# Performance work log

Measured on AMD Instinct MI355X. Metric: run time of the kernel, lower is better.

The kernel has to match this reference:

```python
import jax, jax.numpy as jnp
import numpy as np

B, L, D = 4, 2048, 1024
N, K, H = 8, 1, 128
FG, FA = 4096, 2048
SEP = 1792
SOFTCAP = 50.0
EPS = 1e-6
BIG_NEG = -2.3819763e38


def setup_inputs() -> dict:
    key = jax.random.key(0)
    ks = jax.random.split(key, 16)
    def rnd(k, shape, s=0.02):
        return jax.random.normal(k, shape, dtype=jnp.float32) * s
    return {
        "x": rnd(ks[0], (B, L, D), 1.0),
        "positions": jnp.broadcast_to(jnp.arange(L + 1, dtype=jnp.int32), (B, L + 1)),
        "attn_mask": jnp.ones((B, 1, L, L), dtype=bool),
        "separation_idx": SEP,
        "pre_attn_scale": rnd(ks[1], (D,), 0.1),
        "pre_ffw_scale": rnd(ks[2], (D,), 0.1),
        "g_qw": rnd(ks[3], (N, D, H)),
        "g_kvw": rnd(ks[4], (2, K, D, H)),
        "g_ow": rnd(ks[5], (N, H, D)),
        "a_qw": rnd(ks[6], (N, D, H)),
        "a_kvw": rnd(ks[7], (2, K, D, H)),
        "a_ow": rnd(ks[8], (N, H, D)),
        "g_gate": rnd(ks[9], (2, D, FG)),
        "g_lin": rnd(ks[10], (FG, D)),
        "a_gate": rnd(ks[11], (2, D, FA)),
        "a_lin": rnd(ks[12], (FA, D)),
    }


def rms_norm(x, scale):
    var = jnp.mean(jnp.square(x), axis=-1, keepdims=True)
    return x * jax.lax.rsqrt(var + EPS) * (1.0 + scale)


def apply_rope(x, positions, max_wavelength=10_000.0):
    # x: [B,T,n,H], positions: [B,T]
    hd = x.shape[-1]
    frac = 2.0 * jnp.arange(hd // 2, dtype=jnp.float32) / hd
    timescale = max_wavelength ** frac  # [H/2]
    radians = positions.astype(jnp.float32)[:, :, None, None] / timescale  # [B,T,1,H/2]
    sin, cos = jnp.sin(radians), jnp.cos(radians)
    x1, x2 = jnp.split(x, 2, axis=-1)
    return jnp.concatenate([x1 * cos - x2 * sin, x2 * cos + x1 * sin], axis=-1).astype(x.dtype)


def get_qkv(xn, pos, qw, kvw):
    q = jnp.einsum('btd,ndh->btnh', xn, qw)
    q = apply_rope(q, pos) * (H ** -0.5)  # query_pre_attn_norm == 'rsqrt_head_dim'
    k = apply_rope(jnp.einsum('btd,kdh->btkh', xn, kvw[0]), pos)
    v = jnp.einsum('btd,kdh->btkh', xn, kvw[1])
    return q, k, v


def attention(q, k, v, mask):
    b, t, n, h = q.shape
    kk = k.shape[2]
    g = n // kk
    qg = q.reshape(b, t, kk, g, h)
    logits = jnp.einsum('btkgh,bskh->bkgts', qg, k)
    logits = SOFTCAP * jnp.tanh(logits / SOFTCAP)
    logits = jnp.where(mask[:, :, None], logits, BIG_NEG)  # mask [B,1,T,S] -> [B,1,1,T,S]
    probs = jax.nn.softmax(logits.astype(jnp.float32), axis=-1).astype(q.dtype)
    return jnp.einsum('bkgts,bskh->btkgh', probs, v).reshape(b, t, n, h)


def ffn(x, gate, lin):
    h = jax.nn.gelu(jnp.einsum('btd,df->btf', x, gate[0])) * jnp.einsum('btd,df->btf', x, gate[1])
    return jnp.einsum('btf,fd->btd', h, lin)


def process(attn_out, residual, ffw_scale, gate, lin):
    # post_norms=False, dropout=0: out = mlp(norm(attn + res)) + res (per source)
    h = rms_norm(attn_out + residual, ffw_scale)
    return ffn(h, gate, lin) + residual


def reference(x, positions, attn_mask, separation_idx, pre_attn_scale, pre_ffw_scale,
              g_qw, g_kvw, g_ow, a_qw, a_kvw, a_ow, g_gate, g_lin, a_gate, a_lin):
    sep = separation_idx
    x_g, x_a = x[:, :sep], x[:, sep:]
    n_g = rms_norm(x_g, pre_attn_scale)
    n_a = rms_norm(x_a, pre_attn_scale)
    p_g = positions[:, :sep]
    p_a = positions[:, sep + 1:]
    qg, kg, vg = get_qkv(n_g, p_g, g_qw, g_kvw)
    qa, ka, va = get_qkv(n_a, p_a, a_qw, a_kvw)
    q = jnp.concatenate([qg, qa], axis=1)
    k = jnp.concatenate([kg, ka], axis=1)
    v = jnp.concatenate([vg, va], axis=1)
    attn = attention(q, k, v, attn_mask)  # [B,L,N,H]
    go = jnp.einsum('btnh,nhd->btd', attn[:, :sep], g_ow)
    ao = jnp.einsum('btnh,nhd->btd', attn[:, sep:], a_ow)
    out_g = process(go, x_g, pre_ffw_scale, g_gate, g_lin)
    out_a = process(ao, x_a, pre_ffw_scale, a_gate, a_lin)
    return jnp.concatenate([out_g, out_a], axis=1)
```

## Files before the change

### kernel.cpp

```cpp
#include <hip/hip_runtime.h>
#include <hip/hip_bf16.h>
#include <stdint.h>

typedef short s8b __attribute__((ext_vector_type(8)));
typedef float f4 __attribute__((ext_vector_type(4)));
typedef unsigned short u16t;
typedef unsigned int u32t;

#define AS1 __attribute__((address_space(1)))
#define AS3 __attribute__((address_space(3)))
#define DEVFN static __device__ __forceinline__

DEVFN u16t f2b(float f){ union{ __hip_bfloat16 h; u16t u; } c; c.h = __float2bfloat16(f); return c.u; }

DEVFN float geluf(float x){
  float t = 0.7978845608028654f*(x + 0.044715f*x*x*x);
  t = fminf(fmaxf(t, -15.0f), 15.0f);
  float e = __expf(2.0f*t);
  return 0.5f*x*(1.0f + (e-1.0f)/(e+1.0f));
}
DEVFN float softcapf(float x){
  float t = x*0.02f;
  t = fminf(fmaxf(t, -15.0f), 15.0f);
  float e = __expf(2.0f*t);
  return 50.0f*(e-1.0f)/(e+1.0f);
}

__global__ __launch_bounds__(256) void tpack_k(u16t* __restrict__ dst, const float* __restrict__ src,
                                               int ldsrc, int lddst, int rmul, int roff, int prow,
                                               size_t pstride){
  __shared__ float tile[32][33];
  int z = blockIdx.z;
  const float* s = src + (size_t)z*pstride;
  int f0 = blockIdx.x*32, d0 = blockIdx.y*32;
  int t = threadIdx.x, r = t>>5, c = t&31;
  #pragma unroll
  for(int i=0;i<4;i++)
    tile[r + i*8][c] = s[(size_t)(d0 + r + i*8)*ldsrc + f0 + c];
  __syncthreads();
  int rbase = roff + z*prow;
  #pragma unroll
  for(int i=0;i<4;i++){
    int f = f0 + r + i*8;
    dst[(size_t)(f*rmul + rbase)*lddst + d0 + c] = f2b(tile[c][r + i*8]);
  }
}

__global__ __launch_bounds__(256) void rmsnorm_k(const float* __restrict__ x, const float* __restrict__ sc,
                                                 u16t* __restrict__ out){
  int row = blockIdx.x;
  int tid = threadIdx.x;
  const float* xr = x + (size_t)row*1024;
  float4 v = *(const float4*)(xr + tid*4);
  float s = v.x*v.x + v.y*v.y + v.z*v.z + v.w*v.w;
  #pragma unroll
  for(int off=32; off>=1; off>>=1) s += __shfl_down(s, off);
  __shared__ float ws4[4];
  if((tid & 63) == 0) ws4[tid>>6] = s;
  __syncthreads();
  float tot = ws4[0]+ws4[1]+ws4[2]+ws4[3];
  float r = rsqrtf(tot*(1.0f/1024.0f) + 1e-6f);
  float4 scv = *(const float4*)(sc + tid*4);
  u16t o0 = f2b(v.x*r*(1.0f+scv.x)), o1 = f2b(v.y*r*(1.0f+scv.y));
  u16t o2 = f2b(v.z*r*(1.0f+scv.z)), o3 = f2b(v.w*r*(1.0f+scv.w));
  uint2 pk; pk.x = (u32t)o0 | ((u32t)o1<<16); pk.y = (u32t)o2 | ((u32t)o3<<16);
  *(uint2*)(out + (size_t)row*1024 + tid*4) = pk;
}

__global__ __launch_bounds__(256) void rope_k(const float* __restrict__ qkv, u16t* __restrict__ qb,
                                              u16t* __restrict__ kswz, u16t* __restrict__ vrow){
  int row = blockIdx.x;
  int b = row >> 11, t = row & 2047;
  float pos = (float)(t + (t >= 1792 ? 1 : 0));
  const float* src = qkv + (size_t)row*1280;
  size_t kvbase = ((size_t)b*2048 + t)*128;
  int swz = ((t&7)<<3) ^ (((t>>3)&3)<<4);
  for(int idx = threadIdx.x; idx < 704; idx += 256){
    if(idx < 512){
      int n = idx >> 6, i = idx & 63;
      float inv = exp2f((float)i * -0.20762050593046f);
      float sn, cs; sincosf(pos*inv, &sn, &cs);
      float x1 = src[n*128+i], x2 = src[n*128+i+64];
      const float qs = 0.08838834764831845f;
      qb[(size_t)row*1024 + n*128 + i]      = f2b((x1*cs - x2*sn)*qs);
      qb[(size_t)row*1024 + n*128 + i + 64] = f2b((x2*cs + x1*sn)*qs);
    } else if(idx < 576){
      int i = idx - 512;
      float inv = exp2f((float)i * -0.20762050593046f);
      float sn, cs; sincosf(pos*inv, &sn, &cs);
      float x1 = src[1024+i], x2 = src[1024+i+64];
      kswz[kvbase + (i ^ swz)]        = f2b(x1*cs - x2*sn);
      kswz[kvbase + ((i+64) ^ swz)]   = f2b(x2*cs + x1*sn);
    } else {
      int h = idx - 576;
      vrow[kvbase + h] = f2b(src[1152+h]);
    }
  }
}

__global__ __launch_bounds__(256) void vt_pack_k(const u16t* __restrict__ vrow, u16t* __restrict__ vtswz){
  int blk = blockIdx.x;
  int b = blk >> 5, kt = blk & 31;
  int tid = threadIdx.x;
  const u16t* src = vrow + ((size_t)b*2048 + kt*64)*128;
  #pragma unroll
  for(int it=0; it<4; ++it){
    int o = it*2048 + tid*8;
    int d = o >> 6, kg = o & 63;
    u16t tmp[8];
    #pragma unroll
    for(int j=0;j<8;j++) tmp[j] = src[(size_t)(kg+j)*128 + d];
    *(uint4*)&vtswz[((size_t)b*128 + d)*2048 + kt*64 + (kg ^ ((d&7)<<3))] = *(const uint4*)tmp;
  }
}

struct GemmArgs {
  const u16t* A; int lda;
  const u16t* Bg; const u16t* Ba;
  int K; int ntN; int mode; int amap; int omap; int ep;
  float* outf; u16t* outb; int ldo;
  const float* res;
};

__global__ __launch_bounds__(256) void gemm_k(GemmArgs g){
  __shared__ __align__(16) u16t As[2*128*32];
  __shared__ __align__(16) u16t Bs[2*128*32];
  int bid = blockIdx.x;
  int mt = bid / g.ntN, nt = bid % g.ntN;
  int c0 = mt*128, g0;
  const u16t* B;
  if(g.mode == 0){
    g0 = c0;
    B = ((mt & 15) < 14) ? g.Bg : g.Ba;
  } else if(g.mode == 1){
    int bb = mt/14, t = (mt - bb*14)*128;
    g0 = bb*2048 + t; B = g.Bg;
  } else {
    int bb = mt>>1, t = 1792 + (mt&1)*128;
    g0 = bb*2048 + t; B = g.Bg;
  }
  int arow = g.amap ? g0 : c0;
  int orow = g.omap ? g0 : c0;
  int tid = threadIdx.x, lane = tid & 63, w = tid >> 6, l15 = lane & 15, lg = lane >> 4;
  int wr = w >> 1, wc = w & 1;

  int gsrc = ((tid&3) ^ ((tid>>3)&3))*8;
  const u16t* Ap = g.A + (size_t)(arow + (tid>>2))*g.lda + gsrc;
  const u16t* Bp = B   + (size_t)(nt*128 + (tid>>2))*g.K + gsrc;
  size_t lda64 = (size_t)64*g.lda, ldb64 = (size_t)64*g.K;
  u32t le = tid*8;

  int xr = (lg ^ ((l15>>1)&3))*8;
  int aoff[4], boff[4];
  #pragma unroll
  for(int mi=0;mi<4;mi++) aoff[mi] = (wr*64 + mi*16 + l15)*32 + xr;
  #pragma unroll
  for(int ni=0;ni<4;ni++) boff[ni] = (wc*64 + ni*16 + l15)*32 + xr;

  f4 acc[4][4];
  #pragma unroll
  for(int mi=0;mi<4;mi++)
    #pragma unroll
    for(int ni=0;ni<4;ni++){ f4 z = {0.0f,0.0f,0.0f,0.0f}; acc[mi][ni]=z; }

  auto stagef = [&](int buf, int k0){
    u16t* a = As + buf*4096;
    u16t* b = Bs + buf*4096;
    __builtin_amdgcn_global_load_lds((const AS1 u32t*)(Ap + k0),          (AS3 u32t*)&a[le],        16,0,0);
    __builtin_amdgcn_global_load_lds((const AS1 u32t*)(Ap + k0 + lda64),  (AS3 u32t*)&a[le + 2048], 16,0,0);
    __builtin_amdgcn_global_load_lds((const AS1 u32t*)(Bp + k0),          (AS3 u32t*)&b[le],        16,0,0);
    __builtin_amdgcn_global_load_lds((const AS1 u32t*)(Bp + k0 + ldb64),  (AS3 u32t*)&b[le + 2048], 16,0,0);
  };

  stagef(0, 0);
  __syncthreads();
  int cur = 0;
  for(int k0=0; k0 < g.K; k0 += 32){
    if(k0 + 32 < g.K) stagef(cur^1, k0+32);
    const u16t* as = As + cur*4096;
    const u16t* bs = Bs + cur*4096;
    s8b af[4], bf[4];
    #pragma unroll
    for(int mi=0;mi<4;mi++) af[mi] = *(const s8b*)&as[aoff[mi]];
    #pragma unroll
    for(int ni=0;ni<4;ni++) bf[ni] = *(const s8b*)&bs[boff[ni]];
    #pragma unroll
    for(int mi=0;mi<4;mi++)
      #pragma unroll
      for(int ni=0;ni<4;ni++)
        acc[mi][ni] = __builtin_amdgcn_mfma_f32_16x16x32_bf16(af[mi], bf[ni], acc[mi][ni], 0,0,0);
    __syncthreads();
    cur ^= 1;
  }

  #pragma unroll
  for(int mi=0;mi<4;mi++){
    #pragma unroll
    for(int ni=0;ni<4;ni++){
      int rowb = wr*64 + mi*16 + lg*4;
      int col = nt*128 + wc*64 + ni*16 + l15;
      #pragma unroll
      for(int r=0;r<4;r++){
        float v = acc[mi][ni][r];
        size_t ro = (size_t)(orow + rowb + r);
        if(g.ep == 0){
          g.outf[ro*(size_t)g.ldo + col] = v;
        } else if(g.ep == 1){
          g.outf[ro*(size_t)g.ldo + col] = v + g.res[ro*1024 + col];
        } else {
          float other = __shfl_xor(v, 1);
          if((lane & 1) == 0){
            g.outb[ro*(size_t)g.ldo + (col>>1)] = f2b(geluf(v)*other);
          }
        }
      }
    }
  }
}

__global__ __launch_bounds__(256) void attn_k(const u16t* __restrict__ qb, const u16t* __restrict__ kswz,
                                              const u16t* __restrict__ vtswz, u16t* __restrict__ attnb){
  __shared__ __align__(16) u16t Ks[64*128];
  __shared__ __align__(16) u16t Vt[128*64];
  __shared__ __align__(16) u16t Ps[4*16*72];
  int bid = blockIdx.x;
  int qt = bid & 31, n = (bid>>5)&7, b = bid>>8;
  int tid = threadIdx.x, lane = tid&63, w = tid>>6, l15 = lane&15, lg = lane>>4;
  int q0 = qt*64 + w*16;

  s8b qf[4];
  const u16t* qrow = qb + ((size_t)(b*2048 + q0 + l15)*8 + n)*128;
  #pragma unroll
  for(int kc=0;kc<4;kc++) qf[kc] = *(const s8b*)(qrow + kc*32 + lg*8);

  float lsum[4];
  f4 oacc[8];
  #pragma unroll
  for(int r=0;r<4;r++) lsum[r] = 0.0f;
  #pragma unroll
  for(int db=0;db<8;db++){ f4 z = {0.0f,0.0f,0.0f,0.0f}; oacc[db]=z; }

  const u16t* kbase  = kswz  + (size_t)b*2048*128;
  const u16t* vtbase = vtswz + (size_t)b*128*2048;
  u16t* psw = Ps + w*1152;

  for(int st=0; st<32; ++st){
    const u16t* kt  = kbase  + (size_t)st*64*128;
    const u16t* vtb = vtbase + st*64;
    __syncthreads();
    #pragma unroll
    for(int it=0; it<4; ++it){
      int e = it*2048 + tid*8;
      __builtin_amdgcn_global_load_lds((const AS1 u32t*)(kt + e), (AS3 u32t*)&Ks[e], 16,0,0);
    }
    #pragma unroll
    for(int it=0; it<4; ++it){
      int e = it*2048 + tid*8;
      int d = e >> 6, ko = e & 63;
      __builtin_amdgcn_global_load_lds((const AS1 u32t*)(vtb + (size_t)d*2048 + ko), (AS3 u32t*)&Vt[e], 16,0,0);
    }
    __syncthreads();

    f4 sf[4];
    #pragma unroll
    for(int kb=0;kb<4;kb++){ f4 z = {0.0f,0.0f,0.0f,0.0f}; sf[kb]=z; }
    #pragma unroll
    for(int kb=0;kb<4;kb++){
      int key = kb*16 + l15;
      int swz = ((key&7)<<3) ^ (((key>>3)&3)<<4);
      #pragma unroll
      for(int kc=0;kc<4;kc++){
        s8b kf = *(const s8b*)&Ks[key*128 + ((kc*32 + lg*8) ^ swz)];
        sf[kb] = __builtin_amdgcn_mfma_f32_16x16x32_bf16(qf[kc], kf, sf[kb], 0,0,0);
      }
    }
    #pragma unroll
    for(int r=0;r<4;r++){
      int prow = lg*4 + r;
      #pragma unroll
      for(int kb=0;kb<4;kb++){
        float pv = __expf(softcapf(sf[kb][r]));
        lsum[r] += pv;
        psw[prow*72 + kb*16 + l15] = f2b(pv);
      }
    }
    #pragma unroll
    for(int kc2=0;kc2<2;kc2++){
      s8b pa = *(const s8b*)&psw[l15*72 + kc2*32 + lg*8];
      int koff = (kc2*32 + lg*8) ^ ((l15&7)<<3);
      #pragma unroll
      for(int db=0;db<8;db++){
        s8b vf = *(const s8b*)&Vt[(db*16 + l15)*64 + koff];
        oacc[db] = __builtin_amdgcn_mfma_f32_16x16x32_bf16(pa, vf, oacc[db], 0,0,0);
      }
    }
  }

  float linv[4];
  #pragma unroll
  for(int r=0;r<4;r++){
    float s = lsum[r];
    #pragma unroll
    for(int off=1; off<16; off<<=1) s += __shfl_xor(s, off);
    linv[r] = 1.0f / s;
  }

  #pragma unroll
  for(int db=0;db<8;db++){
    #pragma unroll
    for(int r=0;r<4;r++){
      int qrowi = q0 + lg*4 + r;
      int d = db*16 + l15;
      attnb[(size_t)(b*2048 + qrowi)*1024 + n*128 + d] = f2b(oacc[db][r] * linv[r]);
    }
  }
}

extern "C" void kernel_launch(void* const* d_in, const int* in_sizes, int n_in,
                              void* d_out, int out_size, void* d_ws, size_t ws_size,
                              hipStream_t stream){
  const float* x        = (const float*)d_in[0];
  const float* pre_attn = (const float*)d_in[4];
  const float* pre_ffw  = (const float*)d_in[5];
  const float* g_qw  = (const float*)d_in[6];
  const float* g_kvw = (const float*)d_in[7];
  const float* g_ow  = (const float*)d_in[8];
  const float* a_qw  = (const float*)d_in[9];
  const float* a_kvw = (const float*)d_in[10];
  const float* a_ow  = (const float*)d_in[11];
  const float* g_gate= (const float*)d_in[12];
  const float* g_lin = (const float*)d_in[13];
  const float* a_gate= (const float*)d_in[14];
  const float* a_lin = (const float*)d_in[15];
  float* out = (float*)d_out;
  (void)in_sizes; (void)n_in; (void)out_size; (void)ws_size;

  char* wsp = (char*)d_ws; size_t off = 0;
  auto alloc = [&](size_t b){ void* p = wsp + off; off += (b + 255) & ~(size_t)255; return p; };
  u16t* wqkv_g = (u16t*)alloc((size_t)1280*1024*2);
  u16t* wqkv_a = (u16t*)alloc((size_t)1280*1024*2);
  u16t* wo_g   = (u16t*)alloc((size_t)1024*1024*2);
  u16t* wo_a   = (u16t*)alloc((size_t)1024*1024*2);
  u16t* wg_g   = (u16t*)alloc((size_t)8192*1024*2);
  u16t* wg_a   = (u16t*)alloc((size_t)4096*1024*2);
  u16t* wl_g   = (u16t*)alloc((size_t)1024*4096*2);
  u16t* wl_a   = (u16t*)alloc((size_t)1024*2048*2);
  u16t* xn     = (u16t*)alloc((size_t)8192*1024*2);
  u16t* xn2    = xn;
  char* big    = (char*)alloc((size_t)7168*4096*2);
  float* qkv   = (float*)big;
  float* t1    = (float*)big;
  u16t* hid_g  = (u16t*)big;
  u16t* qb     = (u16t*)alloc((size_t)8192*1024*2);
  u16t* kswz   = (u16t*)alloc((size_t)4*2048*128*2);
  u16t* vrow   = (u16t*)alloc((size_t)4*2048*128*2);
  u16t* vtswz  = (u16t*)alloc((size_t)4*128*2048*2);
  u16t* attnb  = (u16t*)alloc((size_t)8192*1024*2);
  u16t* hid_a  = (u16t*)alloc((size_t)1024*2048*2);

  tpack_k<<<dim3(4,32,8),256,0,stream>>>(wqkv_g, g_qw, 128, 1024, 1, 0, 128, 131072);
  tpack_k<<<dim3(4,32,1),256,0,stream>>>(wqkv_g, g_kvw, 128, 1024, 1, 1024, 0, 0);
  tpack_k<<<dim3(4,32,1),256,0,stream>>>(wqkv_g, g_kvw + 131072, 128, 1024, 1, 1152, 0, 0);
  tpack_k<<<dim3(4,32,8),256,0,stream>>>(wqkv_a, a_qw, 128, 1024, 1, 0, 128, 131072);
  tpack_k<<<dim3(4,32,1),256,0,stream>>>(wqkv_a, a_kvw, 128, 1024, 1, 1024, 0, 0);
  tpack_k<<<dim3(4,32,1),256,0,stream>>>(wqkv_a, a_kvw + 131072, 128, 1024, 1, 1152, 0, 0);
  tpack_k<<<dim3(32,32,1),256,0,stream>>>(wo_g, g_ow, 1024, 1024, 1, 0, 0, 0);
  tpack_k<<<dim3(32,32,1),256,0,stream>>>(wo_a, a_ow, 1024, 1024, 1, 0, 0, 0);
  tpack_k<<<dim3(128,32,2),256,0,stream>>>(wg_g, g_gate, 4096, 1024, 2, 0, 1, (size_t)1024*4096);
  tpack_k<<<dim3(64,32,2),256,0,stream>>>(wg_a, a_gate, 2048, 1024, 2, 0, 1, (size_t)1024*2048);
  tpack_k<<<dim3(32,128,1),256,0,stream>>>(wl_g, g_lin, 1024, 4096, 1, 0, 0, 0);
  tpack_k<<<dim3(32,64,1),256,0,stream>>>(wl_a, a_lin, 1024, 2048, 1, 0, 0, 0);

  rmsnorm_k<<<8192,256,0,stream>>>(x, pre_attn, xn);

  { GemmArgs ga = {xn, 1024, wqkv_g, wqkv_a, 1024, 10, 0,0,0, 0, qkv, nullptr, 1280, nullptr};
    gemm_k<<<64*10,256,0,stream>>>(ga); }
  rope_k<<<8192,256,0,stream>>>(qkv, qb, kswz, vrow);
  vt_pack_k<<<128,256,0,stream>>>(vrow, vtswz);
  attn_k<<<1024,256,0,stream>>>(qb, kswz, vtswz, attnb);
  { GemmArgs ga = {attnb, 1024, wo_g, wo_a, 1024, 8, 0,0,0, 1, t1, nullptr, 1024, x};
    gemm_k<<<64*8,256,0,stream>>>(ga); }
  rmsnorm_k<<<8192,256,0,stream>>>(t1, pre_ffw, xn2);
  { GemmArgs ga = {xn2, 1024, wg_g, nullptr, 1024, 64, 1,1,0, 3, nullptr, hid_g, 4096, nullptr};
    gemm_k<<<56*64,256,0,stream>>>(ga); }
  { GemmArgs ga = {xn2, 1024, wg_a, nullptr, 1024, 32, 2,1,0, 3, nullptr, hid_a, 2048, nullptr};
    gemm_k<<<8*32,256,0,stream>>>(ga); }
  { GemmArgs ga = {hid_g, 4096, wl_g, nullptr, 4096, 8, 1,0,1, 1, out, nullptr, 1024, x};
    gemm_k<<<56*8,256,0,stream>>>(ga); }
  { GemmArgs ga = {hid_a, 2048, wl_a, nullptr, 2048, 8, 2,0,1, 1, out, nullptr, 1024, x};
    gemm_k<<<8*8,256,0,stream>>>(ga); }
}
```

Baseline: 875.3 us.

## Add dedicated 256x256-tile GEMM with LDS double buffering for global gate projection

Replaces the generic gemm_k call for the global-segment gated FFN projection (K=1024, N=8192) with a specialised 512-thread kernel. It uses 256x256 output tiles, double-buffered direct global-to-LDS loads with an XOR swizzle, and a quarter-tile interleaved schedule of loads and MFMAs with priority hints. The fused GELU-gate epilogue is kept. The larger tiles raise operand reuse and the overlap hides load latency, in exchange for 128KB of LDS per block and heavy register use, which limit occupancy. The kernel hardcodes the shapes and the block-to-tile mapping.

After: 873.1 us. About the same (-0.3%).

```diff
diff --git a/kernel.cpp b/kernel.cpp
--- a/kernel.cpp
+++ b/kernel.cpp
@@ -218,6 +218,142 @@
   }
 }
 
+__global__ __launch_bounds__(512, 2) void gemm256_k(const u16t* __restrict__ A,
+                                                    const u16t* __restrict__ Bw,
+                                                    u16t* __restrict__ outb){
+  __shared__ __align__(16) u16t LDS[65536];
+  int bid = blockIdx.x;
+  int wg = (bid & 7)*112 + (bid >> 3);
+  int mt = wg >> 5, nt = wg & 31;
+  int bb = mt / 7;
+  int g0 = bb*2048 + (mt - bb*7)*256;
+  int orow0 = mt*256;
+  int tid = threadIdx.x, lane = tid & 63, w = tid >> 6, l15 = lane & 15, lg = lane >> 4;
+  int wr = w >> 2, wc = w & 3;
+
+  int cg = ((tid&7) ^ ((tid>>3)&7))*8;
+  const u16t* aSrc = A  + (size_t)(g0 + (tid>>3))*1024 + cg;
+  const u16t* bSrc = Bw + (size_t)(nt*256 + (tid>>3))*1024 + cg;
+  u16t* ldsA = &LDS[w*512 + (lane&63)*8];
+  u16t* ldsB = &LDS[32768 + w*512 + (lane&63)*8];
+
+  auto STAGE_A = [&](int kt, int uh){
+    if(kt >= 16) return;
+    const u16t* s0 = aSrc + (size_t)(uh*128)*1024 + kt*64;
+    u16t* d = ldsA + (kt&1)*16384 + uh*8192;
+    __builtin_amdgcn_global_load_lds((const AS1 u32t*)s0,            (AS3 u32t*)d,          16,0,0);
+    __builtin_amdgcn_global_load_lds((const AS1 u32t*)(s0 + 65536),  (AS3 u32t*)(d + 4096), 16,0,0);
+  };
+  auto STAGE_B = [&](int kt, int uh){
+    if(kt >= 16) return;
+    const u16t* s0 = bSrc + (size_t)(uh*128)*1024 + kt*64;
+    u16t* d = ldsB + (kt&1)*16384 + uh*8192;
+    __builtin_amdgcn_global_load_lds((const AS1 u32t*)s0,            (AS3 u32t*)d,          16,0,0);
+    __builtin_amdgcn_global_load_lds((const AS1 u32t*)(s0 + 65536),  (AS3 u32t*)(d + 4096), 16,0,0);
+  };
+
+  int px0 = ((lg)     ^ (l15&7))*8;
+  int px1 = ((4 + lg) ^ (l15&7))*8;
+  int aRow = (wr*128 + l15)*64;
+  int bRow = (wc*64  + l15)*64;
+
+  f4 acc[8][4];
+  #pragma unroll
+  for(int m=0;m<8;m++)
+    #pragma unroll
+    for(int n=0;n<4;n++){ f4 z = {0.0f,0.0f,0.0f,0.0f}; acc[m][n]=z; }
+  s8b afr[4][2], bfr[4][2];
+
+  auto READ_A = [&](int s, int mh){
+    const u16t* base = &LDS[s*16384 + aRow + mh*4096];
+    #pragma unroll
+    for(int m=0;m<4;m++){
+      afr[m][0] = *(const s8b*)(base + m*1024 + px0);
+      afr[m][1] = *(const s8b*)(base + m*1024 + px1);
+    }
+  };
+  auto READ_B = [&](int s, int nh){
+    const u16t* base = &LDS[32768 + s*16384 + bRow + nh*2048];
+    #pragma unroll
+    for(int n=0;n<2;n++){
+      bfr[nh*2+n][0] = *(const s8b*)(base + n*1024 + px0);
+      bfr[nh*2+n][1] = *(const s8b*)(base + n*1024 + px1);
+    }
+  };
+
+  #define MFMAQ(mh, nh)                                                              \
+    __builtin_amdgcn_s_barrier();                                                    \
+    asm volatile("s_waitcnt lgkmcnt(0)" ::: "memory");                               \
+    __builtin_amdgcn_sched_barrier(0);                                               \
+    __builtin_amdgcn_s_setprio(1);                                                   \
+    _Pragma("unroll")                                                                \
+    for(int m=0;m<4;m++)                                                             \
+      _Pragma("unroll")                                                              \
+      for(int n=0;n<2;n++)                                                           \
+        _Pragma("unroll")                                                            \
+        for(int kk=0;kk<2;kk++)                                                      \
+          acc[(mh)*4+m][(nh)*2+n] = __builtin_amdgcn_mfma_f32_16x16x32_bf16(         \
+              afr[m][kk], bfr[(nh)*2+n][kk], acc[(mh)*4+m][(nh)*2+n], 0,0,0);        \
+    __builtin_amdgcn_s_setprio(0);                                                   \
+    __builtin_amdgcn_sched_barrier(0);
+
+  STAGE_A(0,0); STAGE_A(0,1); STAGE_B(0,0); STAGE_B(0,1);
+  STAGE_A(1,0); STAGE_A(1,1);
+  asm volatile("s_waitcnt vmcnt(4)" ::: "memory");
+  __builtin_amdgcn_s_barrier();
+
+  for(int it2=0; it2<8; ++it2){
+    int t = it2*2;
+    READ_B(0,0); READ_A(0,0); STAGE_B(t+1, 0);
+    MFMAQ(0,0)
+    __builtin_amdgcn_s_barrier();
+    READ_B(0,1); STAGE_B(t+1, 1);
+    MFMAQ(0,1)
+    __builtin_amdgcn_s_barrier();
+    READ_A(0,1); STAGE_A(t+2, 0);
+    MFMAQ(1,0)
+    __builtin_amdgcn_s_barrier();
+    STAGE_A(t+2, 1);
+    MFMAQ(1,1)
+    if(it2==7) asm volatile("s_waitcnt vmcnt(0)" ::: "memory");
+    else       asm volatile("s_waitcnt vmcnt(4)" ::: "memory");
+    __builtin_amdgcn_s_barrier();
+    READ_B(1,0); READ_A(1,0); STAGE_B(t+2, 0);
+    MFMAQ(0,0)
+    __builtin_amdgcn_s_barrier();
+    READ_B(1,1); STAGE_B(t+2, 1);
+    MFMAQ(0,1)
+    __builtin_amdgcn_s_barrier();
+    READ_A(1,1); STAGE_A(t+3, 0);
+    MFMAQ(1,0)
+    __builtin_amdgcn_s_barrier();
+    STAGE_A(t+3, 1);
+    MFMAQ(1,1)
+    if(it2==7) asm volatile("s_waitcnt vmcnt(0)" ::: "memory");
+    else       asm volatile("s_waitcnt vmcnt(4)" ::: "memory");
+    __builtin_amdgcn_s_barrier();
+  }
+  #undef MFMAQ
+
+  #pragma unroll
+  for(int mg=0;mg<8;mg++){
+    #pragma unroll
+    for(int n=0;n<4;n++){
+      int rowb = wr*128 + mg*16 + lg*4;
+      int col = nt*256 + wc*64 + n*16 + l15;
+      #pragma unroll
+      for(int r=0;r<4;r++){
+        float v = acc[mg][n][r];
+        float other = __shfl_xor(v, 1);
+        if((lane & 1) == 0){
+          size_t ro = (size_t)(orow0 + rowb + r);
+          outb[ro*4096 + (col>>1)] = f2b(geluf(v)*other);
+        }
+      }
+    }
+  }
+}
+
 __global__ __launch_bounds__(256) void attn_k(const u16t* __restrict__ qb, const u16t* __restrict__ kswz,
                                               const u16t* __restrict__ vtswz, u16t* __restrict__ attnb){
   __shared__ __align__(16) u16t Ks[64*128];
@@ -381,8 +517,7 @@
   { GemmArgs ga = {attnb, 1024, wo_g, wo_a, 1024, 8, 0,0,0, 1, t1, nullptr, 1024, x};
     gemm_k<<<64*8,256,0,stream>>>(ga); }
   rmsnorm_k<<<8192,256,0,stream>>>(t1, pre_ffw, xn2);
-  { GemmArgs ga = {xn2, 1024, wg_g, nullptr, 1024, 64, 1,1,0, 3, nullptr, hid_g, 4096, nullptr};
-    gemm_k<<<56*64,256,0,stream>>>(ga); }
+  gemm256_k<<<896,512,0,stream>>>(xn2, wg_g, hid_g);
   { GemmArgs ga = {xn2, 1024, wg_a, nullptr, 1024, 32, 2,1,0, 3, nullptr, hid_a, 2048, nullptr};
     gemm_k<<<8*32,256,0,stream>>>(ga); }
   { GemmArgs ga = {hid_g, 4096, wl_g, nullptr, 4096, 8, 1,0,1, 1, out, nullptr, 1024, x};
```
